# Kernel tuning notes

Hardware: AMD Instinct MI355X
Metric: run time of the kernel (lower is better)

## Reference

```python
import jax, jax.numpy as jnp
import numpy as np

# Le-ADMM constants (ADMM_Net init values; V_div_mat / R_div_mat are
# precomputed buffers in the torch code using these, not the learned mus)
MU1_0, MU2_0, MU3_0 = 1e-6, 1e-5, 4e-5
TAU_0 = 1e-4
ITERS = 5
BATCH = 8
SENSOR = (540, 960)


def _pad_full(v, sh):
    # zero-pad sensor-size (..., H, W) to full (..., 2H, 2W), centered
    H, W = sh
    pads = [(0, 0)] * (v.ndim - 2) + [(H // 2, H - H // 2), (W // 2, W - W // 2)]
    return jnp.pad(v, pads)


def _crop(v, sh):
    H, W = sh
    return v[..., H // 2:H // 2 + H, W // 2:W // 2 + W]


def _fft2(v):
    return jnp.fft.fft2(jnp.fft.ifftshift(v, axes=(-2, -1)), axes=(-2, -1))


def _ifft2(V):
    return jnp.fft.fftshift(jnp.fft.ifft2(V, axes=(-2, -1)), axes=(-2, -1))


def _Hop(x, Hf):
    return jnp.real(_ifft2(Hf * _fft2(x)))


def _Hadj(x, Hf):
    return jnp.real(_ifft2(jnp.conj(Hf) * _fft2(x)))


def _Psi(x):
    # forward finite differences (circular), vertical and horizontal
    return jnp.roll(x, 1, axis=-2) - x, jnp.roll(x, 1, axis=-1) - x


def _PsiT(uv, uh):
    return (jnp.roll(uv, -1, axis=-2) - uv) + (jnp.roll(uh, -1, axis=-1) - uh)


def _soft_iso(uv, uh, thresh):
    # isotropic soft-threshold on the 2D gradient magnitude
    mag = jnp.sqrt(uv * uv + uh * uh)
    mult = jnp.maximum(mag - thresh, 0.0) / jnp.maximum(mag, 1e-12)
    return uv * mult, uh * mult


def setup_inputs() -> dict:
    key = jax.random.key(0)
    k1, k2 = jax.random.split(key)
    x = jax.random.uniform(k1, (BATCH,) + SENSOR, dtype=jnp.float32)
    h = jax.random.uniform(k2, SENSOR, dtype=jnp.float32)
    h = h / jnp.linalg.norm(h)  # normalized PSF
    ones = jnp.ones((ITERS,), jnp.float32)
    return {
        "x": x,
        "h": h,
        "mu1": ones * MU1_0,
        "mu2": ones * MU2_0,
        "mu3": ones * MU3_0,
        "tau": ones * TAU_0,
    }


def reference(x, h, mu1, mu2, mu3, tau):
    sh = h.shape  # sensor size (H, W)
    fullH, fullW = 2 * sh[0], 2 * sh[1]

    Hf = _fft2(_pad_full(h[None], sh))[0]  # (2H, 2W) complex
    CtC = _pad_full(jnp.ones((1,) + sh, x.dtype), sh)[0]
    V_div = 1.0 / (CtC + MU1_0)
    lap = jnp.zeros((fullH, fullW), x.dtype)
    lap = (lap.at[0, 0].set(4.0).at[0, 1].set(-1.0).at[1, 0].set(-1.0)
           .at[0, -1].set(-1.0).at[-1, 0].set(-1.0))
    PsiTPsi = jnp.abs(jnp.fft.fft2(lap))
    R_div = 1.0 / (MU1_0 * jnp.abs(Hf) ** 2 + MU2_0 * PsiTPsi + MU3_0)

    Cty = _pad_full(x, sh)  # (B, 2H, 2W)
    zfull = jnp.zeros((x.shape[0], fullH, fullW), x.dtype)

    out = zfull
    for i in range(ITERS):
        # forward() calls admm.restValues() every iteration, so all ADMM state
        # (X, U, V, W, alphas) is zero at the start of each iteration: each
        # iteration is one ADMM step from zero state; output keeps the last.
        X, a1, a2v, a2h, a3 = zfull, zfull, zfull, zfull, zfull
        pv, ph = _Psi(X)
        Uv, Uh = _soft_iso(pv + a2v / mu2[i], ph + a2h / mu2[i], tau[i] / mu2[i])
        V = V_div * (a1 + mu1[i] * _Hop(X, Hf) + Cty)
        W = jnp.maximum(a3 / mu3[i] + X, 0.0)
        r = ((mu3[i] * W - a3)
             + _PsiT(mu2[i] * Uv - a2v, mu2[i] * Uh - a2h)
             + _Hadj(mu1[i] * V - a1, Hf))
        out = jnp.real(_ifft2(R_div * _fft2(r)))
    return _crop(out, sh)
```

## Files before the change

### kernel.cpp

```cpp
#include <hip/hip_runtime.h>


#define PI2 6.2831853071795864f

__device__ __forceinline__ float2 cadd(float2 a, float2 b){ return make_float2(a.x+b.x, a.y+b.y); }
__device__ __forceinline__ float2 csub(float2 a, float2 b){ return make_float2(a.x-b.x, a.y-b.y); }
__device__ __forceinline__ float2 cmul(float2 a, float2 b){ return make_float2(a.x*b.x - a.y*b.y, a.x*b.y + a.y*b.x); }
__device__ __forceinline__ float4 pk(float2 a, float2 b){ return make_float4(a.x,a.y,b.x,b.y); }

__device__ __forceinline__ int IDX(int a){ return a + (a >> 4); }
#define IDXSZ(n) ((n) + ((n) >> 4))
__device__ __forceinline__ int IDXP(int a){ return a + ((a >> 5) << 1); }
#define IDXPSZ(n) ((n) + (((n) >> 5) << 1) + 4)

__device__ __forceinline__ void ldp(const float2* __restrict__ b, int pos,
                                    float2& v0, float2& v1){
    const float4 t = *(const float4*)&b[IDXP(2*pos)];
    v0 = make_float2(t.x,t.y); v1 = make_float2(t.z,t.w);
}
__device__ __forceinline__ void stp(float2* __restrict__ b, int pos,
                                    float2 v0, float2 v1){
    *(float4*)&b[IDXP(2*pos)] = pk(v0, v1);
}

template<int DIR>
__device__ __forceinline__ void dft3(float2 x0, float2 x1, float2 x2,
                                     float2& y0, float2& y1, float2& y2)
{
    constexpr float s3 = (float)DIR * 0.8660254037844386f;
    float2 t = cadd(x1, x2), u = csub(x1, x2);
    float2 m = make_float2(x0.x - 0.5f*t.x, x0.y - 0.5f*t.y);
    float2 iu = make_float2(-s3*u.y, s3*u.x);
    y0 = cadd(x0, t); y1 = cadd(m, iu); y2 = csub(m, iu);
}

template<int DIR>
__device__ __forceinline__ void dft4(float2 a0, float2 a1, float2 a2, float2 a3,
                                     float2& b0, float2& b1, float2& b2, float2& b3)
{
    float2 t0 = cadd(a0,a2), t1 = csub(a0,a2), t2 = cadd(a1,a3), t3 = csub(a1,a3);
    float2 j3 = make_float2(-(float)DIR*t3.y, (float)DIR*t3.x);
    b0 = cadd(t0,t2); b2 = csub(t0,t2); b1 = cadd(t1,j3); b3 = csub(t1,j3);
}

template<int DIR>
__device__ __forceinline__ void dft6(const float2 a[6], float2 b[6])
{
    float2 e0,e1,e2,o0,o1,o2;
    dft3<DIR>(a[0],a[2],a[4], e0,e1,e2);
    dft3<DIR>(a[1],a[3],a[5], o0,o1,o2);
    constexpr float s3 = (float)DIR * 0.8660254037844386f;
    float2 w1 = make_float2( 0.5f, s3);
    float2 w2 = make_float2(-0.5f, s3);
    float2 t1 = cmul(w1,o1), t2 = cmul(w2,o2);
    b[0]=cadd(e0,o0); b[3]=csub(e0,o0);
    b[1]=cadd(e1,t1); b[4]=csub(e1,t1);
    b[2]=cadd(e2,t2); b[5]=csub(e2,t2);
}

template<int DIR>
__device__ __forceinline__ void dft8(const float2 a[8], float2 b[8])
{
    float2 e0,e1,e2,e3,o0,o1,o2,o3;
    dft4<DIR>(a[0],a[2],a[4],a[6], e0,e1,e2,e3);
    dft4<DIR>(a[1],a[3],a[5],a[7], o0,o1,o2,o3);
    constexpr float c = 0.70710678118654752f;
    float2 w1 = make_float2( c, (float)DIR*c);
    float2 w3 = make_float2(-c, (float)DIR*c);
    float2 t1 = cmul(w1,o1);
    float2 t2 = make_float2(-(float)DIR*o2.y, (float)DIR*o2.x);
    float2 t3 = cmul(w3,o3);
    b[0]=cadd(e0,o0); b[4]=csub(e0,o0);
    b[1]=cadd(e1,t1); b[5]=csub(e1,t1);
    b[2]=cadd(e2,t2); b[6]=csub(e2,t2);
    b[3]=cadd(e3,t3); b[7]=csub(e3,t3);
}

template<int DIR>
__device__ __forceinline__ void dft5(const float2 a[5], float2 b[5])
{
    constexpr float C1 = 0.30901699437494742f, S1c = 0.9510565162951535f;
    constexpr float C2 = -0.8090169943749475f, S2c = 0.5877852522924731f;
    float2 t1 = cadd(a[1],a[4]), t2 = cadd(a[2],a[3]), d1 = csub(a[1],a[4]), d2 = csub(a[2],a[3]);
    float2 m1 = make_float2(a[0].x + C1*t1.x + C2*t2.x, a[0].y + C1*t1.y + C2*t2.y);
    float2 m2 = make_float2(a[0].x + C2*t1.x + C1*t2.x, a[0].y + C2*t1.y + C1*t2.y);
    float2 e1 = make_float2(S1c*d1.x + S2c*d2.x, S1c*d1.y + S2c*d2.y);
    float2 e2 = make_float2(S2c*d1.x - S1c*d2.x, S2c*d1.y - S1c*d2.y);
    float2 ie1 = make_float2(-(float)DIR*e1.y, (float)DIR*e1.x);
    float2 ie2 = make_float2(-(float)DIR*e2.y, (float)DIR*e2.x);
    b[0] = make_float2(a[0].x + t1.x + t2.x, a[0].y + t1.y + t2.y);
    b[1] = cadd(m1, ie1); b[4] = csub(m1, ie1);
    b[2] = cadd(m2, ie2); b[3] = csub(m2, ie2);
}

template<int DIR, int R, int NCUR, int S>
__device__ __forceinline__ void mid_stage(const float2* __restrict__ src,
                                          float2* __restrict__ dst, int tid)
{
    constexpr int M  = NCUR / R;
    constexpr int NB = M * S;
    constexpr float STEP = (float)DIR * PI2 / (float)NCUR;
    for (int i = tid; i < NB; i += 256) {
        const int p = i / S;
        float2 a[R], b[R];
        #pragma unroll
        for (int t = 0; t < R; ++t) a[t] = src[IDX(i + S*M*t)];
        if constexpr (R == 6) dft6<DIR>(a,b); else dft8<DIR>(a,b);
        float sv, cv; __sincosf(STEP * (float)p, &sv, &cv);
        float2 w1 = make_float2(cv, sv), w = w1;
        b[1] = cmul(b[1], w);
        #pragma unroll
        for (int u = 2; u < R; ++u) { w = cmul(w, w1); b[u] = cmul(b[u], w); }
        const int ob = (i - p*S) + S*(R*p);
        #pragma unroll
        for (int u = 0; u < R; ++u) dst[IDX(ob + S*u)] = b[u];
    }
}

template<int DIR, int NCUR, int SC>
__device__ __forceinline__ void mid_pair(const float2* __restrict__ src,
                                         float2* __restrict__ dst, int tid)
{
    constexpr int NB = 180;
    constexpr float STEP = (float)DIR * PI2 / (float)NCUR;
    for (int ic = tid; ic < NB; ic += 256) {
        const int p = ic / SC;
        float2 a0[6], a1[6], b0[6], b1[6];
        #pragma unroll
        for (int t = 0; t < 6; ++t) ldp(src, ic + NB*t, a0[t], a1[t]);
        dft6<DIR>(a0,b0); dft6<DIR>(a1,b1);
        float sv, cv; __sincosf(STEP*(float)p, &sv, &cv);
        float2 w1 = make_float2(cv,sv), w = w1;
        b0[1]=cmul(b0[1],w); b1[1]=cmul(b1[1],w);
        #pragma unroll
        for (int u = 2; u < 6; ++u){ w = cmul(w,w1); b0[u]=cmul(b0[u],w); b1[u]=cmul(b1[u],w); }
        const int ob = (ic - p*SC) + SC*6*p;
        #pragma unroll
        for (int u = 0; u < 6; ++u) stp(dst, ob + SC*u, b0[u], b1[u]);
    }
}

__device__ __forceinline__ void col_s1_fwd_pair(const float2* __restrict__ g, int c0,
                                                float2* __restrict__ bA, int tid)
{
    constexpr float STEP = -PI2 / 1080.0f;
    const float2 z = make_float2(0.f,0.f);
    const float4* gc = (const float4*)(g + c0);
    for (int p = tid; p < 180; p += 256) {
        float2 a0[6], a1[6], b0[6], b1[6];
        a0[0]=a0[5]=a1[0]=a1[5]=z;
        if (p >= 90) { float4 t = gc[(p-90)*960]; a0[1]=make_float2(t.x,t.y); a1[1]=make_float2(t.z,t.w); }
        else         { a0[1]=a1[1]=z; }
        { float4 t = gc[(p+90)*960];  a0[2]=make_float2(t.x,t.y); a1[2]=make_float2(t.z,t.w); }
        { float4 t = gc[(p+270)*960]; a0[3]=make_float2(t.x,t.y); a1[3]=make_float2(t.z,t.w); }
        if (p < 90)  { float4 t = gc[(p+450)*960]; a0[4]=make_float2(t.x,t.y); a1[4]=make_float2(t.z,t.w); }
        else         { a0[4]=a1[4]=z; }
        dft6<-1>(a0,b0); dft6<-1>(a1,b1);
        float sv, cv; __sincosf(STEP*(float)p, &sv, &cv);
        float2 w1 = make_float2(cv,sv), w = w1;
        b0[1]=cmul(b0[1],w); b1[1]=cmul(b1[1],w);
        #pragma unroll
        for (int u = 2; u < 6; ++u){ w = cmul(w,w1); b0[u]=cmul(b0[u],w); b1[u]=cmul(b1[u],w); }
        #pragma unroll
        for (int u = 0; u < 6; ++u) stp(bA, 6*p + u, b0[u], b1[u]);
    }
}

__device__ __forceinline__ void fused5K5_pair(const float2* __restrict__ src,
                                              float2* __restrict__ dst,
                                              const float4* __restrict__ KI,
                                              int cpair, int tid)
{
    constexpr float STEP = PI2 / 1080.0f;
    const float4* Kc = KI + cpair*1080;
    for (int p = tid; p < 216; p += 256) {
        float2 a0[5],a1[5],s0[5],s1[5],d0[5],d1[5];
        #pragma unroll
        for (int u = 0; u < 5; ++u) ldp(src, p + 216*u, a0[u], a1[u]);
        dft5<-1>(a0,s0); dft5<-1>(a1,s1);
        #pragma unroll
        for (int u = 0; u < 5; ++u) {
            float4 kk = Kc[p + 216*u];
            s0[u] = cmul(s0[u], make_float2(kk.x,kk.y));
            s1[u] = cmul(s1[u], make_float2(kk.z,kk.w));
        }
        dft5<1>(s0,d0); dft5<1>(s1,d1);
        float sv, cv; __sincosf(STEP*(float)p, &sv, &cv);
        float2 w1 = make_float2(cv,sv), w = w1;
        d0[1]=cmul(d0[1],w); d1[1]=cmul(d1[1],w);
        #pragma unroll
        for (int u = 2; u < 5; ++u){ w = cmul(w,w1); d0[u]=cmul(d0[u],w); d1[u]=cmul(d1[u],w); }
        #pragma unroll
        for (int u = 0; u < 5; ++u) stp(dst, 5*p + u, d0[u], d1[u]);
    }
}

__device__ __forceinline__ void fin6_crop_pair(const float2* __restrict__ src,
                                               float2* __restrict__ Zp,
                                               int c0, int tid)
{
    float4* gc = (float4*)(Zp + c0);
    for (int m = tid; m < 180; m += 256) {
        float2 a0[6],a1[6],b0[6],b1[6];
        #pragma unroll
        for (int t = 0; t < 6; ++t) ldp(src, m + 180*t, a0[t], a1[t]);
        dft6<1>(a0,b0); dft6<1>(a1,b1);
        gc[(m+270)*960] = pk(b0[0], b1[0]);
        if (m < 90)  gc[(m+450)*960] = pk(b0[1], b1[1]);
        if (m >= 90) gc[(m-90)*960]  = pk(b0[4], b1[4]);
        gc[(m+90)*960]  = pk(b0[5], b1[5]);
    }
}


template<bool HASB>
__device__ __forceinline__ void row_s1_fwd(const float* __restrict__ xa,
                                           const float* __restrict__ xb,
                                           float2* __restrict__ bA, int tid)
{
    constexpr float STEP = -PI2 / 1920.0f;
    const float2 z = make_float2(0.f,0.f);
    for (int p = tid; p < 240; p += 256) {
        float2 a[8], b[8];
        a[0]=z; a[1]=z; a[6]=z; a[7]=z;
        a[2] = make_float2(xa[p],     HASB ? xb[p]     : 0.f);
        a[3] = make_float2(xa[p+240], HASB ? xb[p+240] : 0.f);
        a[4] = make_float2(xa[p+480], HASB ? xb[p+480] : 0.f);
        a[5] = make_float2(xa[p+720], HASB ? xb[p+720] : 0.f);
        dft8<-1>(a,b);
        float sv, cv; __sincosf(STEP * (float)p, &sv, &cv);
        float2 w1 = make_float2(cv, sv), w = w1;
        b[1] = cmul(b[1], w);
        #pragma unroll
        for (int u = 2; u < 8; ++u) { w = cmul(w, w1); b[u] = cmul(b[u], w); }
        #pragma unroll
        for (int u = 0; u < 8; ++u) bA[IDX(8*p + u)] = b[u];
    }
}

__device__ __forceinline__ void row_s1_inv(const float2* __restrict__ Zp,
                                           float2* __restrict__ bA, int tid)
{
    constexpr float STEP = PI2 / 1920.0f;
    for (int p = tid; p < 240; p += 256) {
        float2 a[8], b[8];
        #pragma unroll
        for (int t = 0; t < 8; ++t) a[t] = Zp[p + 240*t];
        dft8<1>(a,b);
        float sv, cv; __sincosf(STEP * (float)p, &sv, &cv);
        float2 w1 = make_float2(cv, sv), w = w1;
        b[1] = cmul(b[1], w);
        #pragma unroll
        for (int u = 2; u < 8; ++u) { w = cmul(w, w1); b[u] = cmul(b[u], w); }
        #pragma unroll
        for (int u = 0; u < 8; ++u) bA[IDX(8*p + u)] = b[u];
    }
}

template<int DIR>
__device__ __forceinline__ void row_fin5_store(const float2* __restrict__ src,
                                               float2* __restrict__ gdst, int tid)
{
    for (int q = tid; q < 384; q += 256) {
        float2 a[5], b[5];
        #pragma unroll
        for (int u = 0; u < 5; ++u) a[u] = src[IDX(q + 384*u)];
        dft5<DIR>(a,b);
        #pragma unroll
        for (int u = 0; u < 5; ++u) gdst[q + 384*u] = b[u];
    }
}


__global__ __launch_bounds__(256,5) void k_row_fft_h(const float* __restrict__ h,
                                                     float2* __restrict__ Hrow)
{
    __shared__ float2 bA[IDXSZ(1920)], bB[IDXSZ(1920)];
    const int tid = threadIdx.x, r = blockIdx.x;
    row_s1_fwd<false>(h + r*960, nullptr, bA, tid); __syncthreads();
    mid_stage<-1,8,240, 8>(bA, bB, tid); __syncthreads();
    mid_stage<-1,6, 30,64>(bB, bA, tid); __syncthreads();
    row_fin5_store<-1>(bA, Hrow + r*1920, tid);
}

__global__ __launch_bounds__(256,4) void k_col_fft_h_buildK(const float2* __restrict__ Hrow,
                                                            const float* __restrict__ mu1,
                                                            float4* __restrict__ KI)
{
    __shared__ float2 bA[IDXPSZ(2160)], bB[IDXPSZ(2160)];
    const int tid = threadIdx.x;
    const int xcd = blockIdx.x & 7, idx = blockIdx.x >> 3;
    const int cpair = xcd*120 + idx, c0 = cpair*2;
    col_s1_fwd_pair(Hrow, c0, bA, tid);  __syncthreads();
    mid_pair<-1,180, 6>(bA, bB, tid);    __syncthreads();
    mid_pair<-1, 30,36>(bB, bA, tid);    __syncthreads();
    const float sc = mu1[4] / ((1.0f + 1e-6f) * 2073600.0f);
    const float cos0 = __cosf(PI2 * (float)(c0  ) * (1.0f/1920.0f));
    const float cos1 = __cosf(PI2 * (float)(c0+1) * (1.0f/1920.0f));
    float4* Kc = KI + cpair*1080;
    for (int p = tid; p < 216; p += 256) {
        float2 a0[5],a1[5],b0[5],b1[5];
        #pragma unroll
        for (int u = 0; u < 5; ++u) ldp(bA, p + 216*u, a0[u], a1[u]);
        dft5<-1>(a0,b0); dft5<-1>(a1,b1);
        #pragma unroll
        for (int u = 0; u < 5; ++u) {
            const int k = p + 216*u;
            const float cosk = __cosf(PI2 * (float)k * (1.0f/1080.0f));
            float m0 = b0[u].x*b0[u].x + b0[u].y*b0[u].y;
            float m1 = b1[u].x*b1[u].x + b1[u].y*b1[u].y;
            float f0 = sc / (1e-6f*m0 + 1e-5f*(4.0f - 2.0f*cosk - 2.0f*cos0) + 4e-5f);
            float f1 = sc / (1e-6f*m1 + 1e-5f*(4.0f - 2.0f*cosk - 2.0f*cos1) + 4e-5f);
            Kc[k] = make_float4(f0*b0[u].x, -f0*b0[u].y, f1*b1[u].x, -f1*b1[u].y);
        }
    }
}

__global__ __launch_bounds__(256,5) void k_row_fft_x(const float* __restrict__ x,
                                                     float2* __restrict__ Z)
{
    __shared__ float2 bA[IDXSZ(1920)], bB[IDXSZ(1920)];
    const int tid = threadIdx.x;
    const int p = blockIdx.x / 540;
    const int r = blockIdx.x % 540;
    row_s1_fwd<true>(x + ((2*p)*540 + r)*960, x + ((2*p+1)*540 + r)*960, bA, tid);
    __syncthreads();
    mid_stage<-1,8,240, 8>(bA, bB, tid); __syncthreads();
    mid_stage<-1,6, 30,64>(bB, bA, tid); __syncthreads();
    row_fin5_store<-1>(bA, Z + (p*540 + r)*1920, tid);
}

__global__ __launch_bounds__(256,4) void k_col_fused(float2* __restrict__ Z,
                                                     const float4* __restrict__ KI)
{
    __shared__ float2 bA[IDXPSZ(2160)], bB[IDXPSZ(2160)];
    const int tid = threadIdx.x;
    const int xcd = blockIdx.x & 7, idx = blockIdx.x >> 3;
    const int pp  = idx / 120;
    const int cpair = xcd*120 + (idx - pp*120), c0 = cpair*2;
    float2* Zp = Z + pp*540*1920;
    col_s1_fwd_pair(Zp, c0, bA, tid);      __syncthreads();
    mid_pair<-1,180, 6>(bA, bB, tid);      __syncthreads();
    mid_pair<-1, 30,36>(bB, bA, tid);      __syncthreads();
    fused5K5_pair(bA, bB, KI, cpair, tid); __syncthreads();
    mid_pair< 1,216, 5>(bB, bA, tid);      __syncthreads();
    mid_pair< 1, 36,30>(bA, bB, tid);      __syncthreads();
    fin6_crop_pair(bB, Zp, c0, tid);
}

__global__ __launch_bounds__(256,5) void k_row_ifft_out(const float2* __restrict__ Z,
                                                        float* __restrict__ out)
{
    __shared__ float2 bA[IDXSZ(1920)], bB[IDXSZ(1920)];
    const int tid = threadIdx.x;
    const int p = blockIdx.x / 540;
    const int r = blockIdx.x % 540;
    row_s1_inv(Z + (p*540 + r)*1920, bA, tid); __syncthreads();
    mid_stage<1,8,240, 8>(bA, bB, tid); __syncthreads();
    mid_stage<1,6, 30,64>(bB, bA, tid); __syncthreads();
    float* oa = out + ((2*p)*540 + r)*960;
    float* ob = out + ((2*p+1)*540 + r)*960;
    for (int q = tid; q < 384; q += 256) {
        float2 a[5], b[5];
        #pragma unroll
        for (int u = 0; u < 5; ++u) a[u] = bA[IDX(q + 384*u)];
        dft5<1>(a,b);
        oa[q+480] = b[0].x; ob[q+480] = b[0].y;
        if (q < 96)   { oa[q+864] = b[1].x; ob[q+864] = b[1].y; }
        if (q >= 288) { oa[q-288] = b[3].x; ob[q-288] = b[3].y; }
        oa[q+96]  = b[4].x; ob[q+96]  = b[4].y;
    }
}

extern "C" void kernel_launch(void* const* d_in, const int* in_sizes, int n_in,
                              void* d_out, int out_size, void* d_ws, size_t ws_size,
                              hipStream_t stream)
{
    (void)in_sizes; (void)n_in; (void)out_size; (void)ws_size;
    const float* x   = (const float*)d_in[0];
    const float* h   = (const float*)d_in[1];
    const float* mu1 = (const float*)d_in[2];
    float*       out = (float*)d_out;

    float4* KI   = (float4*)d_ws;
    float2* Z    = (float2*)d_ws + 2*960*1080;
    float2* Hrow = Z;

    k_row_fft_h       <<<540,    256, 0, stream>>>(h, Hrow);
    k_col_fft_h_buildK<<<960,    256, 0, stream>>>(Hrow, mu1, KI);
    k_row_fft_x       <<<4*540,  256, 0, stream>>>(x, Z);
    k_col_fused       <<<3840,   256, 0, stream>>>(Z, KI);
    k_row_ifft_out    <<<4*540,  256, 0, stream>>>(Z, out);
}
```

Measured before the change: 87.18 us.

## Use higher-radix 10/12/9 factorization for column FFT to cut LDS passes

The 1080-point column FFT/IFFT pair in k_col_fused is refactored from 6·6·30/5 style radix stages into radix-10, radix-12 and a fused radix-9 kernel-multiply stage. This cuts the number of shared-memory passes and __syncthreads barriers from seven stages to five. The trade-off is much larger per-thread register arrays (two 12-point complex sets plus temporaries), which could hurt occupancy under launch_bounds(256,4). Each stage also now uses only 108–120 of the 256 threads, leaving many lanes idle.

```diff
diff --git a/kernel.cpp b/kernel.cpp
--- a/kernel.cpp
+++ b/kernel.cpp
@@ -93,6 +93,62 @@
     b[2] = cadd(m2, ie2); b[3] = csub(m2, ie2);
 }
 
+template<int DIR>
+__device__ __forceinline__ void dft9(const float2 a[9], float2 b[9])
+{
+    float2 C0[3], C1[3], C2[3];
+    dft3<DIR>(a[0],a[3],a[6], C0[0],C0[1],C0[2]);
+    dft3<DIR>(a[1],a[4],a[7], C1[0],C1[1],C1[2]);
+    dft3<DIR>(a[2],a[5],a[8], C2[0],C2[1],C2[2]);
+    const float2 w91 = make_float2(0.7660444431189780f, (float)DIR*0.6427876096865393f);
+    const float2 w92 = make_float2(0.1736481776669304f, (float)DIR*0.9848077530122081f);
+    const float2 w94 = make_float2(-0.9396926207859084f, (float)DIR*0.3420201433256687f);
+    C1[1]=cmul(C1[1],w91); C1[2]=cmul(C1[2],w92);
+    C2[1]=cmul(C2[1],w92); C2[2]=cmul(C2[2],w94);
+    dft3<DIR>(C0[0],C1[0],C2[0], b[0],b[3],b[6]);
+    dft3<DIR>(C0[1],C1[1],C2[1], b[1],b[4],b[7]);
+    dft3<DIR>(C0[2],C1[2],C2[2], b[2],b[5],b[8]);
+}
+
+template<int DIR>
+__device__ __forceinline__ void dft10(const float2 a[10], float2 b[10])
+{
+    float2 ae[5] = {a[0],a[2],a[4],a[6],a[8]};
+    float2 ao[5] = {a[1],a[3],a[5],a[7],a[9]};
+    float2 E[5], O[5];
+    dft5<DIR>(ae, E); dft5<DIR>(ao, O);
+    const float2 w1 = make_float2( 0.8090169943749475f, (float)DIR*0.5877852522924731f);
+    const float2 w2 = make_float2( 0.3090169943749474f, (float)DIR*0.9510565162951535f);
+    const float2 w3 = make_float2(-0.3090169943749474f, (float)DIR*0.9510565162951535f);
+    const float2 w4 = make_float2(-0.8090169943749475f, (float)DIR*0.5877852522924731f);
+    float2 t1 = cmul(O[1],w1), t2 = cmul(O[2],w2), t3 = cmul(O[3],w3), t4 = cmul(O[4],w4);
+    b[0]=cadd(E[0],O[0]); b[5]=csub(E[0],O[0]);
+    b[1]=cadd(E[1],t1);   b[6]=csub(E[1],t1);
+    b[2]=cadd(E[2],t2);   b[7]=csub(E[2],t2);
+    b[3]=cadd(E[3],t3);   b[8]=csub(E[3],t3);
+    b[4]=cadd(E[4],t4);   b[9]=csub(E[4],t4);
+}
+
+template<int DIR>
+__device__ __forceinline__ void dft12(const float2 a[12], float2 b[12])
+{
+    float2 C0[4], C1[4], C2[4];
+    dft4<DIR>(a[0],a[3],a[6],a[9],  C0[0],C0[1],C0[2],C0[3]);
+    dft4<DIR>(a[1],a[4],a[7],a[10], C1[0],C1[1],C1[2],C1[3]);
+    dft4<DIR>(a[2],a[5],a[8],a[11], C2[0],C2[1],C2[2],C2[3]);
+    const float2 w121 = make_float2(0.8660254037844386f, (float)DIR*0.5f);
+    const float2 w122 = make_float2(0.5f, (float)DIR*0.8660254037844386f);
+    const float2 w124 = make_float2(-0.5f, (float)DIR*0.8660254037844386f);
+    C1[1]=cmul(C1[1],w121); C1[2]=cmul(C1[2],w122);
+    C1[3]=make_float2(-(float)DIR*C1[3].y, (float)DIR*C1[3].x);
+    C2[1]=cmul(C2[1],w122); C2[2]=cmul(C2[2],w124);
+    C2[3]=make_float2(-C2[3].x, -C2[3].y);
+    dft3<DIR>(C0[0],C1[0],C2[0], b[0],b[4],b[8]);
+    dft3<DIR>(C0[1],C1[1],C2[1], b[1],b[5],b[9]);
+    dft3<DIR>(C0[2],C1[2],C2[2], b[2],b[6],b[10]);
+    dft3<DIR>(C0[3],C1[3],C2[3], b[3],b[7],b[11]);
+}
+
 template<int DIR, int R, int NCUR, int S>
 __device__ __forceinline__ void mid_stage(const float2* __restrict__ src,
                                           float2* __restrict__ dst, int tid)
@@ -137,6 +193,29 @@
         const int ob = (ic - p*SC) + SC*6*p;
         #pragma unroll
         for (int u = 0; u < 6; ++u) stp(dst, ob + SC*u, b0[u], b1[u]);
+    }
+}
+
+template<int DIR, int NCUR, int SC>
+__device__ __forceinline__ void mid12_pair(const float2* __restrict__ src,
+                                           float2* __restrict__ dst, int tid)
+{
+    constexpr int NB = (NCUR/12)*SC;
+    constexpr float STEP = (float)DIR * PI2 / (float)NCUR;
+    for (int ic = tid; ic < NB; ic += 256) {
+        const int p = ic / SC;
+        float2 a0[12], a1[12], b0[12], b1[12];
+        #pragma unroll
+        for (int t = 0; t < 12; ++t) ldp(src, ic + NB*t, a0[t], a1[t]);
+        dft12<DIR>(a0,b0); dft12<DIR>(a1,b1);
+        float sv, cv; __sincosf(STEP*(float)p, &sv, &cv);
+        float2 w1 = make_float2(cv,sv), w = w1;
+        b0[1]=cmul(b0[1],w); b1[1]=cmul(b1[1],w);
+        #pragma unroll
+        for (int u = 2; u < 12; ++u){ w = cmul(w,w1); b0[u]=cmul(b0[u],w); b1[u]=cmul(b1[u],w); }
+        const int ob = (ic - p*SC) + SC*12*p;
+        #pragma unroll
+        for (int u = 0; u < 12; ++u) stp(dst, ob + SC*u, b0[u], b1[u]);
     }
 }
 
@@ -166,49 +245,79 @@
     }
 }
 
-__device__ __forceinline__ void fused5K5_pair(const float2* __restrict__ src,
+__device__ __forceinline__ void col_s1_fwd10_pair(const float2* __restrict__ g, int c0,
+                                                  float2* __restrict__ bA, int tid)
+{
+    constexpr float STEP = -PI2 / 1080.0f;
+    const float2 z = make_float2(0.f,0.f);
+    const float4* gc = (const float4*)(g + c0);
+    for (int p = tid; p < 108; p += 256) {
+        float2 a0[10], a1[10], b0[10], b1[10];
+        a0[0]=a0[1]=a0[8]=a0[9]=z; a1[0]=a1[1]=a1[8]=a1[9]=z;
+        if (p >= 54) { float4 t = gc[(p-54)*960]; a0[2]=make_float2(t.x,t.y); a1[2]=make_float2(t.z,t.w); }
+        else         { a0[2]=a1[2]=z; }
+        { float4 t = gc[(p+54)*960];  a0[3]=make_float2(t.x,t.y); a1[3]=make_float2(t.z,t.w); }
+        { float4 t = gc[(p+162)*960]; a0[4]=make_float2(t.x,t.y); a1[4]=make_float2(t.z,t.w); }
+        { float4 t = gc[(p+270)*960]; a0[5]=make_float2(t.x,t.y); a1[5]=make_float2(t.z,t.w); }
+        { float4 t = gc[(p+378)*960]; a0[6]=make_float2(t.x,t.y); a1[6]=make_float2(t.z,t.w); }
+        if (p < 54)  { float4 t = gc[(p+486)*960]; a0[7]=make_float2(t.x,t.y); a1[7]=make_float2(t.z,t.w); }
+        else         { a0[7]=a1[7]=z; }
+        dft10<-1>(a0,b0); dft10<-1>(a1,b1);
+        float sv, cv; __sincosf(STEP*(float)p, &sv, &cv);
+        float2 w1 = make_float2(cv,sv), w = w1;
+        b0[1]=cmul(b0[1],w); b1[1]=cmul(b1[1],w);
+        #pragma unroll
+        for (int u = 2; u < 10; ++u){ w = cmul(w,w1); b0[u]=cmul(b0[u],w); b1[u]=cmul(b1[u],w); }
+        #pragma unroll
+        for (int u = 0; u < 10; ++u) stp(bA, 10*p + u, b0[u], b1[u]);
+    }
+}
+
+__device__ __forceinline__ void fused9K9_pair(const float2* __restrict__ src,
                                               float2* __restrict__ dst,
                                               const float4* __restrict__ KI,
                                               int cpair, int tid)
 {
     constexpr float STEP = PI2 / 1080.0f;
     const float4* Kc = KI + cpair*1080;
-    for (int p = tid; p < 216; p += 256) {
-        float2 a0[5],a1[5],s0[5],s1[5],d0[5],d1[5];
-        #pragma unroll
-        for (int u = 0; u < 5; ++u) ldp(src, p + 216*u, a0[u], a1[u]);
-        dft5<-1>(a0,s0); dft5<-1>(a1,s1);
-        #pragma unroll
-        for (int u = 0; u < 5; ++u) {
-            float4 kk = Kc[p + 216*u];
+    for (int q = tid; q < 120; q += 256) {
+        float2 a0[9], a1[9], s0[9], s1[9], d0[9], d1[9];
+        #pragma unroll
+        for (int u = 0; u < 9; ++u) ldp(src, q + 120*u, a0[u], a1[u]);
+        dft9<-1>(a0,s0); dft9<-1>(a1,s1);
+        #pragma unroll
+        for (int u = 0; u < 9; ++u) {
+            float4 kk = Kc[q + 120*u];
             s0[u] = cmul(s0[u], make_float2(kk.x,kk.y));
             s1[u] = cmul(s1[u], make_float2(kk.z,kk.w));
         }
-        dft5<1>(s0,d0); dft5<1>(s1,d1);
-        float sv, cv; __sincosf(STEP*(float)p, &sv, &cv);
+        dft9<1>(s0,d0); dft9<1>(s1,d1);
+        float sv, cv; __sincosf(STEP*(float)q, &sv, &cv);
         float2 w1 = make_float2(cv,sv), w = w1;
         d0[1]=cmul(d0[1],w); d1[1]=cmul(d1[1],w);
         #pragma unroll
-        for (int u = 2; u < 5; ++u){ w = cmul(w,w1); d0[u]=cmul(d0[u],w); d1[u]=cmul(d1[u],w); }
-        #pragma unroll
-        for (int u = 0; u < 5; ++u) stp(dst, 5*p + u, d0[u], d1[u]);
-    }
-}
-
-__device__ __forceinline__ void fin6_crop_pair(const float2* __restrict__ src,
-                                               float2* __restrict__ Zp,
-                                               int c0, int tid)
+        for (int u = 2; u < 9; ++u){ w = cmul(w,w1); d0[u]=cmul(d0[u],w); d1[u]=cmul(d1[u],w); }
+        #pragma unroll
+        for (int u = 0; u < 9; ++u) stp(dst, 9*q + u, d0[u], d1[u]);
+    }
+}
+
+__device__ __forceinline__ void fin10_crop_pair(const float2* __restrict__ src,
+                                                float2* __restrict__ Zp,
+                                                int c0, int tid)
 {
     float4* gc = (float4*)(Zp + c0);
-    for (int m = tid; m < 180; m += 256) {
-        float2 a0[6],a1[6],b0[6],b1[6];
-        #pragma unroll
-        for (int t = 0; t < 6; ++t) ldp(src, m + 180*t, a0[t], a1[t]);
-        dft6<1>(a0,b0); dft6<1>(a1,b1);
-        gc[(m+270)*960] = pk(b0[0], b1[0]);
-        if (m < 90)  gc[(m+450)*960] = pk(b0[1], b1[1]);
-        if (m >= 90) gc[(m-90)*960]  = pk(b0[4], b1[4]);
-        gc[(m+90)*960]  = pk(b0[5], b1[5]);
+    for (int q = tid; q < 108; q += 256) {
+        float2 a0[10], a1[10], b0[10], b1[10];
+        #pragma unroll
+        for (int u = 0; u < 10; ++u) ldp(src, q + 108*u, a0[u], a1[u]);
+        dft10<1>(a0,b0); dft10<1>(a1,b1);
+        gc[(q+270)*960] = pk(b0[0], b1[0]);
+        gc[(q+378)*960] = pk(b0[1], b1[1]);
+        if (q < 54)  gc[(q+486)*960] = pk(b0[2], b1[2]);
+        if (q >= 54) gc[(q-54)*960]  = pk(b0[7], b1[7]);
+        gc[(q+54)*960]  = pk(b0[8], b1[8]);
+        gc[(q+162)*960] = pk(b0[9], b1[9]);
     }
 }
 
@@ -339,13 +448,11 @@
     const int pp  = idx / 120;
     const int cpair = xcd*120 + (idx - pp*120), c0 = cpair*2;
     float2* Zp = Z + pp*540*1920;
-    col_s1_fwd_pair(Zp, c0, bA, tid);      __syncthreads();
-    mid_pair<-1,180, 6>(bA, bB, tid);      __syncthreads();
-    mid_pair<-1, 30,36>(bB, bA, tid);      __syncthreads();
-    fused5K5_pair(bA, bB, KI, cpair, tid); __syncthreads();
-    mid_pair< 1,216, 5>(bB, bA, tid);      __syncthreads();
-    mid_pair< 1, 36,30>(bA, bB, tid);      __syncthreads();
-    fin6_crop_pair(bB, Zp, c0, tid);
+    col_s1_fwd10_pair(Zp, c0, bA, tid);    __syncthreads();
+    mid12_pair<-1,108,10>(bA, bB, tid);    __syncthreads();
+    fused9K9_pair(bB, bA, KI, cpair, tid); __syncthreads();
+    mid12_pair< 1,120, 9>(bA, bB, tid);    __syncthreads();
+    fin10_crop_pair(bB, Zp, c0, tid);
 }
 
 __global__ __launch_bounds__(256,5) void k_row_ifft_out(const float2* __restrict__ Z,
```

Measured after the change: 101.4 us. 16.3% more time.
